# Performance work log

Hardware: AMD Instinct MI355X
Metric: run time of the kernel (lower is better)

Reference implementation:

```python
import jax, jax.numpy as jnp
import numpy as np
import math

K = 3
IN_CH = 512
OUT_CH = 512
W_DIM = 512
B = 16
HW = 64
LR_MUL = 1.0


def setup_inputs() -> dict:
    key = jax.random.key(0)
    k1, k2, k3, k4 = jax.random.split(key, 4)
    x = jax.random.normal(k1, (B, HW, HW, IN_CH), dtype=jnp.float32)
    w_latents = jax.random.normal(k2, (B, W_DIM), dtype=jnp.float32)
    w = jax.random.normal(k3, (K, K, IN_CH, OUT_CH), dtype=jnp.float32)  # init_std = 1/lr_mul = 1
    b = jnp.zeros((OUT_CH,), dtype=jnp.float32)
    fc_w = jax.random.normal(k4, (W_DIM, IN_CH), dtype=jnp.float32)
    fc_b = jnp.zeros((IN_CH,), dtype=jnp.float32)
    return {"x": x, "w_latents": w_latents, "w": w, "b": b, "fc_w": fc_w, "fc_b": fc_b}


def reference(x, w_latents, w, b, fc_w, fc_b):
    # equalized-LR runtime coefficients (gain=1)
    conv_coef = LR_MUL / math.sqrt(K * K * IN_CH)
    fc_coef = LR_MUL / math.sqrt(W_DIM)

    batch, H, W_, Cin = x.shape
    x_nchw = jnp.transpose(x, (0, 3, 1, 2))  # [B, Cin, H, W]

    weight = w * conv_coef  # [k,k,in,out]
    # style modulation: fully_connected (no lrelu) + 1
    s = w_latents @ (fc_w * fc_coef) + fc_b * LR_MUL + 1.0  # [B, in]

    # per-sample modulated weights [B,k,k,in,out]
    ww = weight[None] * s[:, None, None, :, None]
    # demodulation
    d = jax.lax.rsqrt(jnp.sum(jnp.square(ww), axis=(1, 2, 3)) + 1e-8)  # [B, out]
    ww = ww * d[:, None, None, None, :]

    # fused_modconv: grouped conv with groups = batch
    x_g = x_nchw.reshape(1, batch * Cin, H, W_)
    w_g = jnp.transpose(ww, (1, 2, 3, 0, 4)).reshape(K, K, Cin, batch * OUT_CH)
    y = jax.lax.conv_general_dilated(
        x_g, w_g,
        window_strides=(1, 1),
        padding='SAME',
        dimension_numbers=('NCHW', 'HWIO', 'NCHW'),
        feature_group_count=batch,
    )  # [1, B*out, H, W]
    y = y.reshape(batch, OUT_CH, H, W_)
    y = jnp.transpose(y, (0, 2, 3, 1))  # NHWC
    y = y + (b * LR_MUL)
    return y
```

## Files before the change

### kernel.cpp

```cpp
#include <hip/hip_runtime.h>
#include <hip/hip_bf16.h>

#define IN_CH 512
#define OUT_CH 512
#define W_DIM 512
#define BATCH 16
#define HWDIM 64
#define PADW 66

static constexpr float CONV_COEF = 0.014731391274719739f;
static constexpr float FC_COEF   = 0.044194173824159216f;

typedef __bf16 bf16x8 __attribute__((ext_vector_type(8)));
typedef float  f32x4  __attribute__((ext_vector_type(4)));

typedef __attribute__((address_space(1))) void gvoid;
typedef __attribute__((address_space(3))) void lvoid;

__device__ __forceinline__ void async_cp16(const void* g, void* l) {
    __builtin_amdgcn_global_load_lds((gvoid*)g, (lvoid*)l, 16, 0, 0);
}

__device__ __forceinline__ ushort f2bf(float f) {
    union { float f; unsigned u; } un; un.f = f;
    unsigned u = un.u;
    return (ushort)((u + 0x7fffu + ((u >> 16) & 1u)) >> 16);
}

__global__ void k_halo(ushort* __restrict__ xs) {
    int b = blockIdx.y;
    int pidx = blockIdx.x * 4 + (threadIdx.x >> 6);
    int ch = threadIdx.x & 63;
    int h, w;
    if (pidx < 66)       { h = 0;          w = pidx; }
    else if (pidx < 132) { h = 65;         w = pidx - 66; }
    else if (pidx < 196) { h = pidx - 131; w = 0; }
    else                 { h = pidx - 195; w = 65; }
    size_t base = (((size_t)(b * PADW + h)) * PADW + w) * IN_CH + ch * 8;
    uint4 z = {0u, 0u, 0u, 0u};
    *(uint4*)(xs + base) = z;
}

__global__ void k_style(const float* __restrict__ wl, const float* __restrict__ fcw,
                        const float* __restrict__ fcb, float* __restrict__ s) {
    int b = blockIdx.x;
    int i = blockIdx.y * 128 + threadIdx.x;
    __shared__ float lw[W_DIM];
    for (int j = threadIdx.x; j < W_DIM; j += 128) lw[j] = wl[b * W_DIM + j];
    __syncthreads();
    float acc = 0.f;
#pragma unroll 8
    for (int j = 0; j < W_DIM; ++j) acc += lw[j] * fcw[(size_t)j * IN_CH + i];
    s[b * IN_CH + i] = acc * FC_COEF + fcb[i] + 1.0f;
}

__global__ void k_xs(const float* __restrict__ x, const float* __restrict__ s,
                     ushort* __restrict__ xs) {
    int t = blockIdx.x * blockDim.x + threadIdx.x;
    int pix = t >> 7;
    int c = (t & 127) << 2;
    int b = pix >> 12;
    int hw = pix & 4095;
    int h = hw >> 6, w = hw & 63;
    float4 xv = ((const float4*)x)[t];
    float4 sv = ((const float4*)(s + b * IN_CH))[t & 127];
    ushort4 o;
    o.x = f2bf(xv.x * sv.x);
    o.y = f2bf(xv.y * sv.y);
    o.z = f2bf(xv.z * sv.z);
    o.w = f2bf(xv.w * sv.w);
    size_t dst = (((size_t)(b * PADW + h + 1)) * PADW + (w + 1)) * IN_CH + c;
    *(ushort4*)(xs + dst) = o;
}

__global__ void k_wt(const float* __restrict__ w, ushort* __restrict__ wT) {
    __shared__ float tile[32][33];
    int kk = blockIdx.z;
    const float* src = w + (size_t)kk * IN_CH * OUT_CH;
    ushort* dst = wT + (size_t)kk * IN_CH * OUT_CH;
    int i0 = blockIdx.y * 32;
    int o0 = blockIdx.x * 32;
    int tx = threadIdx.x, ty = threadIdx.y;
#pragma unroll
    for (int rr = 0; rr < 32; rr += 8)
        tile[ty + rr][tx] = src[(size_t)(i0 + ty + rr) * OUT_CH + o0 + tx];
    __syncthreads();
#pragma unroll
    for (int rr = 0; rr < 32; rr += 8)
        dst[(size_t)(o0 + ty + rr) * IN_CH + i0 + tx] = f2bf(tile[tx][ty + rr]);
}

__global__ void k_a2(const float* __restrict__ w, float* __restrict__ a2) {
    int n = blockIdx.x * blockDim.x + threadIdx.x;
    float sum = 0.f;
#pragma unroll
    for (int kk = 0; kk < 9; ++kk) {
        float v = w[(size_t)kk * (IN_CH * OUT_CH) + n];
        sum += v * v;
    }
    a2[n] = sum;
}

__global__ void k_dmod(const float* __restrict__ s, const float* __restrict__ a2,
                       float* __restrict__ dmod) {
    int b = blockIdx.x;
    int o = blockIdx.y * 128 + threadIdx.x;
    __shared__ float s2[IN_CH];
    for (int i = threadIdx.x; i < IN_CH; i += 128) {
        float v = s[b * IN_CH + i];
        s2[i] = v * v;
    }
    __syncthreads();
    float acc = 0.f;
#pragma unroll 8
    for (int i = 0; i < IN_CH; ++i) acc += s2[i] * a2[(size_t)i * OUT_CH + o];
    dmod[b * OUT_CH + o] = rsqrtf(acc * CONV_COEF * CONV_COEF + 1e-8f);
}


__device__ __forceinline__ int aoff_of(int t) {
    int kk = t >> 3;
    int c0 = (t & 7) << 6;
    int kh = (kk >= 6) ? 2 : ((kk >= 3) ? 1 : 0);
    int kw = kk - kh * 3;
    return (kh * PADW + kw) * IN_CH + c0;
}

__device__ __forceinline__ int boff_of(int t) {
    int kk = t >> 3;
    int c0 = (t & 7) << 6;
    return kk * (IN_CH * OUT_CH) + c0;
}

__device__ __forceinline__ void stage8(const ushort* gA, const ushort* gB,
                                       ushort* dA, ushort* dB) {
#pragma unroll
    for (int i = 0; i < 4; ++i) {
        async_cp16(gA + i * (PADW * IN_CH), dA + i * 4096);
        async_cp16(gB + i * (64 * IN_CH), dB + i * 4096);
    }
}

__device__ __forceinline__ void compute_step(
        const ushort* aB0, const ushort* aB1,
        const ushort* bB0, const ushort* bB1,
        f32x4 (&acc)[8][4]) {
#pragma unroll
    for (int ks = 0; ks < 2; ++ks) {
        const ushort* aB = ks ? aB1 : aB0;
        const ushort* bB = ks ? bB1 : bB0;
        bf16x8 bv[4];
#pragma unroll
        for (int j = 0; j < 4; ++j) bv[j] = *(const bf16x8*)(bB + j * 1024);
#pragma unroll
        for (int mh = 0; mh < 2; ++mh) {
            bf16x8 av[4];
#pragma unroll
            for (int f = 0; f < 4; ++f)
                av[f] = *(const bf16x8*)(aB + (mh * 4 + f) * 1024);
            __builtin_amdgcn_s_setprio(1);
#pragma unroll
            for (int i = 0; i < 4; ++i)
#pragma unroll
                for (int j = 0; j < 4; ++j)
                    acc[mh * 4 + i][j] = __builtin_amdgcn_mfma_f32_16x16x32_bf16(
                        av[i], bv[j], acc[mh * 4 + i][j], 0, 0, 0);
            __builtin_amdgcn_s_setprio(0);
        }
    }
}

__global__ __launch_bounds__(512, 2) void k_conv(
    const ushort* __restrict__ xs, const ushort* __restrict__ wT,
    const float* __restrict__ dmod, const float* __restrict__ bias,
    float* __restrict__ out) {
    __shared__ __align__(16) ushort smem[4][16384];

    const int tid = threadIdx.x;
    const int wave = tid >> 6;
    const int lane = tid & 63;
    const int srow = tid >> 3;
    const int lc = (tid & 7) ^ (srow & 7);

    const int wg = (blockIdx.x & 7) * 64 + (blockIdx.x >> 3);
    const int nt = wg >> 8;
    const int mt = wg & 255;
    const int b  = mt >> 4;
    const int h0 = (mt & 15) << 2;
    const int n0 = nt << 8;

    const ushort* gA0 = xs + (((size_t)(b * PADW + h0)) * PADW + srow) * IN_CH + lc * 8;
    const ushort* gB0 = wT + ((size_t)(n0 + srow)) * IN_CH + lc * 8;

    ushort* dA[2] = { &smem[0][wave * 512], &smem[2][wave * 512] };
    ushort* dB[2] = { &smem[1][wave * 512], &smem[3][wave * 512] };

    const int rlane = lane & 15;
    const int q = lane >> 4;
    const int wm = wave >> 2;
    const int wn = wave & 3;
    const int pc0 = ((q + 0) ^ (rlane & 7)) * 8;
    const int pc1 = ((q + 4) ^ (rlane & 7)) * 8;

    const ushort* aR[2][2];
    const ushort* bR[2][2];
#pragma unroll
    for (int bf = 0; bf < 2; ++bf) {
        aR[bf][0] = &smem[bf * 2][(wm * 128 + rlane) * 64 + pc0];
        aR[bf][1] = &smem[bf * 2][(wm * 128 + rlane) * 64 + pc1];
        bR[bf][0] = &smem[bf * 2 + 1][(wn * 64 + rlane) * 64 + pc0];
        bR[bf][1] = &smem[bf * 2 + 1][(wn * 64 + rlane) * 64 + pc1];
    }

    f32x4 acc[8][4];
#pragma unroll
    for (int i = 0; i < 8; ++i)
#pragma unroll
        for (int j = 0; j < 4; ++j) {
            f32x4 z = {0.f, 0.f, 0.f, 0.f};
            acc[i][j] = z;
        }

    stage8(gA0 + aoff_of(0), gB0 + boff_of(0), dA[0], dB[0]);

#pragma unroll 1
    for (int t = 0; t < 72; t += 2) {
        stage8(gA0 + aoff_of(t + 1), gB0 + boff_of(t + 1), dA[1], dB[1]);
        asm volatile("s_waitcnt vmcnt(8)" ::: "memory");
        __builtin_amdgcn_s_barrier();
        asm volatile("" ::: "memory");
        compute_step(aR[0][0], aR[0][1], bR[0][0], bR[0][1], acc);
        asm volatile("" ::: "memory");
        __builtin_amdgcn_s_barrier();
        asm volatile("" ::: "memory");

        if (t + 2 < 72) {
            stage8(gA0 + aoff_of(t + 2), gB0 + boff_of(t + 2), dA[0], dB[0]);
            asm volatile("s_waitcnt vmcnt(8)" ::: "memory");
        } else {
            asm volatile("s_waitcnt vmcnt(0)" ::: "memory");
        }
        __builtin_amdgcn_s_barrier();
        asm volatile("" ::: "memory");
        compute_step(aR[1][0], aR[1][1], bR[1][0], bR[1][1], acc);
        asm volatile("" ::: "memory");
        __builtin_amdgcn_s_barrier();
        asm volatile("" ::: "memory");
    }

#pragma unroll
    for (int j = 0; j < 4; ++j) {
        const int n = n0 + wn * 64 + j * 16 + rlane;
        const float scale = dmod[b * OUT_CH + n] * CONV_COEF;
        const float bv2 = bias[n];
#pragma unroll
        for (int i = 0; i < 8; ++i) {
#pragma unroll
            for (int e = 0; e < 4; ++e) {
                const int m = wm * 128 + i * 16 + q * 4 + e;
                const int h = h0 + (m >> 6);
                const int w = m & 63;
                out[(((size_t)(b * HWDIM + h)) * HWDIM + w) * OUT_CH + n] =
                    acc[i][j][e] * scale + bv2;
            }
        }
    }
}

extern "C" void kernel_launch(void* const* d_in, const int* in_sizes, int n_in,
                              void* d_out, int out_size, void* d_ws, size_t ws_size,
                              hipStream_t stream) {
    const float* x    = (const float*)d_in[0];
    const float* wl   = (const float*)d_in[1];
    const float* w    = (const float*)d_in[2];
    const float* bias = (const float*)d_in[3];
    const float* fcw  = (const float*)d_in[4];
    const float* fcb  = (const float*)d_in[5];
    float* out = (float*)d_out;

    char* ws = (char*)d_ws;
    const size_t XS_BYTES = (size_t)BATCH * PADW * PADW * IN_CH * 2;
    const size_t WT_BYTES = (size_t)9 * IN_CH * OUT_CH * 2;
    ushort* xs   = (ushort*)ws;
    ushort* wT   = (ushort*)(ws + XS_BYTES);
    float*  s    = (float*)(ws + XS_BYTES + WT_BYTES);
    float*  dmod = s + BATCH * IN_CH;
    float*  a2   = dmod + BATCH * OUT_CH;

    k_halo<<<dim3(65, BATCH), 256, 0, stream>>>(xs);
    k_style<<<dim3(BATCH, 4), 128, 0, stream>>>(wl, fcw, fcb, s);
    k_xs<<<(BATCH * HWDIM * HWDIM * IN_CH / 4) / 256, 256, 0, stream>>>(x, s, xs);
    k_wt<<<dim3(16, 16, 9), dim3(32, 8), 0, stream>>>(w, wT);
    k_a2<<<(IN_CH * OUT_CH) / 256, 256, 0, stream>>>(w, a2);
    k_dmod<<<dim3(BATCH, 4), 128, 0, stream>>>(s, a2, dmod);
    k_conv<<<512, 512, 0, stream>>>(xs, wT, dmod, bias, out);
}
```

Baseline: 564.2 us.

## Interleave async global-to-LDS staging with split MFMA phases in conv mainloop

Restructures the implicit-GEMM main loop into four barrier-separated phases per K-tile. Each phase issues its LDS fragment reads, and the next tile's A or B global-to-LDS copies are spread across the first two phases, in the style of an HipKittens-like 8-wave ping-pong schedule. The intent is to overlap memory traffic with MFMA work more finely and to keep fewer fragments live. In exchange it adds more barriers per tile and waits for all outstanding loads (vmcnt(0)) at the end of every step, which could serialize the prefetch.

```diff
diff --git a/kernel.cpp b/kernel.cpp
--- a/kernel.cpp
+++ b/kernel.cpp
@@ -132,42 +132,69 @@
     return kk * (IN_CH * OUT_CH) + c0;
 }
 
-__device__ __forceinline__ void stage8(const ushort* gA, const ushort* gB,
-                                       ushort* dA, ushort* dB) {
-#pragma unroll
-    for (int i = 0; i < 4; ++i) {
-        async_cp16(gA + i * (PADW * IN_CH), dA + i * 4096);
-        async_cp16(gB + i * (64 * IN_CH), dB + i * 4096);
-    }
-}
-
-__device__ __forceinline__ void compute_step(
-        const ushort* aB0, const ushort* aB1,
-        const ushort* bB0, const ushort* bB1,
-        f32x4 (&acc)[8][4]) {
-#pragma unroll
-    for (int ks = 0; ks < 2; ++ks) {
-        const ushort* aB = ks ? aB1 : aB0;
-        const ushort* bB = ks ? bB1 : bB0;
-        bf16x8 bv[4];
-#pragma unroll
-        for (int j = 0; j < 4; ++j) bv[j] = *(const bf16x8*)(bB + j * 1024);
-#pragma unroll
-        for (int mh = 0; mh < 2; ++mh) {
-            bf16x8 av[4];
-#pragma unroll
-            for (int f = 0; f < 4; ++f)
-                av[f] = *(const bf16x8*)(aB + (mh * 4 + f) * 1024);
-            __builtin_amdgcn_s_setprio(1);
-#pragma unroll
-            for (int i = 0; i < 4; ++i)
-#pragma unroll
-                for (int j = 0; j < 4; ++j)
-                    acc[mh * 4 + i][j] = __builtin_amdgcn_mfma_f32_16x16x32_bf16(
-                        av[i], bv[j], acc[mh * 4 + i][j], 0, 0, 0);
-            __builtin_amdgcn_s_setprio(0);
-        }
-    }
+__device__ __forceinline__ void bar() {
+    asm volatile("" ::: "memory");
+    __builtin_amdgcn_s_barrier();
+    asm volatile("" ::: "memory");
+}
+
+#define MFMA16(AV, MH)                                                        \
+    __builtin_amdgcn_s_setprio(1);                                            \
+    _Pragma("unroll")                                                         \
+    for (int i = 0; i < 4; ++i)                                               \
+        _Pragma("unroll")                                                     \
+        for (int j = 0; j < 4; ++j)                                           \
+            acc[(MH)*4 + i][j] = __builtin_amdgcn_mfma_f32_16x16x32_bf16(     \
+                AV[i], bv[j], acc[(MH)*4 + i][j], 0, 0, 0);                   \
+    __builtin_amdgcn_s_setprio(0);
+
+__device__ __forceinline__ void step4(
+    const ushort* __restrict__ aBase, const ushort* __restrict__ bBase,
+    int pc0, int pc1,
+    const ushort* __restrict__ gA, const ushort* __restrict__ gB,
+    ushort* __restrict__ dA, ushort* __restrict__ dB,
+    bool doStage, f32x4 (&acc)[8][4])
+{
+    bf16x8 av[4], bv[4];
+
+#pragma unroll
+    for (int f = 0; f < 4; ++f) bv[f] = *(const bf16x8*)(bBase + f * 1024 + pc0);
+#pragma unroll
+    for (int f = 0; f < 4; ++f) av[f] = *(const bf16x8*)(aBase + f * 1024 + pc0);
+    if (doStage) {
+#pragma unroll
+        for (int i = 0; i < 4; ++i)
+            async_cp16(gA + i * (PADW * IN_CH), dA + i * 4096);
+    }
+    bar();
+    MFMA16(av, 0)
+    bar();
+
+#pragma unroll
+    for (int f = 0; f < 4; ++f) av[f] = *(const bf16x8*)(aBase + 4096 + f * 1024 + pc0);
+    if (doStage) {
+#pragma unroll
+        for (int i = 0; i < 4; ++i)
+            async_cp16(gB + i * (64 * IN_CH), dB + i * 4096);
+    }
+    bar();
+    MFMA16(av, 1)
+    bar();
+
+#pragma unroll
+    for (int f = 0; f < 4; ++f) bv[f] = *(const bf16x8*)(bBase + f * 1024 + pc1);
+#pragma unroll
+    for (int f = 0; f < 4; ++f) av[f] = *(const bf16x8*)(aBase + f * 1024 + pc1);
+    bar();
+    MFMA16(av, 0)
+    bar();
+
+#pragma unroll
+    for (int f = 0; f < 4; ++f) av[f] = *(const bf16x8*)(aBase + 4096 + f * 1024 + pc1);
+    bar();
+    MFMA16(av, 1)
+    asm volatile("s_waitcnt vmcnt(0)" ::: "memory");
+    bar();
 }
 
 __global__ __launch_bounds__(512, 2) void k_conv(
@@ -202,15 +229,14 @@
     const int pc0 = ((q + 0) ^ (rlane & 7)) * 8;
     const int pc1 = ((q + 4) ^ (rlane & 7)) * 8;
 
-    const ushort* aR[2][2];
-    const ushort* bR[2][2];
-#pragma unroll
-    for (int bf = 0; bf < 2; ++bf) {
-        aR[bf][0] = &smem[bf * 2][(wm * 128 + rlane) * 64 + pc0];
-        aR[bf][1] = &smem[bf * 2][(wm * 128 + rlane) * 64 + pc1];
-        bR[bf][0] = &smem[bf * 2 + 1][(wn * 64 + rlane) * 64 + pc0];
-        bR[bf][1] = &smem[bf * 2 + 1][(wn * 64 + rlane) * 64 + pc1];
-    }
+    const ushort* aBase[2] = {
+        &smem[0][(wm * 128 + rlane) * 64],
+        &smem[2][(wm * 128 + rlane) * 64],
+    };
+    const ushort* bBase[2] = {
+        &smem[1][(wn * 64 + rlane) * 64],
+        &smem[3][(wn * 64 + rlane) * 64],
+    };
 
     f32x4 acc[8][4];
 #pragma unroll
@@ -221,31 +247,22 @@
             acc[i][j] = z;
         }
 
-    stage8(gA0 + aoff_of(0), gB0 + boff_of(0), dA[0], dB[0]);
+#pragma unroll
+    for (int i = 0; i < 4; ++i) {
+        async_cp16(gA0 + aoff_of(0) + i * (PADW * IN_CH), dA[0] + i * 4096);
+        async_cp16(gB0 + boff_of(0) + i * (64 * IN_CH), dB[0] + i * 4096);
+    }
+    asm volatile("s_waitcnt vmcnt(0)" ::: "memory");
+    bar();
 
 #pragma unroll 1
     for (int t = 0; t < 72; t += 2) {
-        stage8(gA0 + aoff_of(t + 1), gB0 + boff_of(t + 1), dA[1], dB[1]);
-        asm volatile("s_waitcnt vmcnt(8)" ::: "memory");
-        __builtin_amdgcn_s_barrier();
-        asm volatile("" ::: "memory");
-        compute_step(aR[0][0], aR[0][1], bR[0][0], bR[0][1], acc);
-        asm volatile("" ::: "memory");
-        __builtin_amdgcn_s_barrier();
-        asm volatile("" ::: "memory");
-
-        if (t + 2 < 72) {
-            stage8(gA0 + aoff_of(t + 2), gB0 + boff_of(t + 2), dA[0], dB[0]);
-            asm volatile("s_waitcnt vmcnt(8)" ::: "memory");
-        } else {
-            asm volatile("s_waitcnt vmcnt(0)" ::: "memory");
-        }
-        __builtin_amdgcn_s_barrier();
-        asm volatile("" ::: "memory");
-        compute_step(aR[1][0], aR[1][1], bR[1][0], bR[1][1], acc);
-        asm volatile("" ::: "memory");
-        __builtin_amdgcn_s_barrier();
-        asm volatile("" ::: "memory");
+        step4(aBase[0], bBase[0], pc0, pc1,
+              gA0 + aoff_of(t + 1), gB0 + boff_of(t + 1),
+              dA[1], dB[1], true, acc);
+        step4(aBase[1], bBase[1], pc0, pc1,
+              gA0 + aoff_of(t + 2), gB0 + boff_of(t + 2),
+              dA[0], dB[0], (t + 2 < 72), acc);
     }
 
 #pragma unroll
```

New measurement: 549.5 us. 1.03x faster.
